# Kernel optimization log

Hardware: AMD Instinct MI355X
Metric: run time of the kernel (lower is better)

The kernel has to match this reference:

```python
import jax, jax.numpy as jnp
import numpy as np

LOOKUP_WINDOW = 101
OUTPUT_DIM = 128
NUM_BINS = 512


def setup_inputs() -> dict:
    key = jax.random.key(0)
    k1, k2 = jax.random.split(key)
    frames = jax.random.randint(k1, (16, 100, 27, 48, 3), 0, 256, dtype=jnp.int32)
    fc_w = jax.random.normal(k2, (LOOKUP_WINDOW, OUTPUT_DIM), dtype=jnp.float32) * 0.05
    fc_b = jnp.zeros((OUTPUT_DIM,), dtype=jnp.float32)
    return {"frames": frames, "fc_w": fc_w, "fc_b": fc_b}


def _color_histograms(frames):
    # frames: [B, T, H, W, 3] int32 in [0, 256)
    B, T, H, W, C = frames.shape
    f = frames.reshape(B * T, H * W, 3)
    R, G, Bc = f[:, :, 0], f[:, :, 1], f[:, :, 2]
    # 3 bits per channel -> 512 bins
    bins = ((R >> 5) << 6) + ((G >> 5) << 3) + (Bc >> 5)  # [BT, HW]
    frame_prefix = (jnp.arange(B * T, dtype=jnp.int32) << 9)[:, None]
    ids = (bins + frame_prefix).reshape(-1)
    hist = jax.ops.segment_sum(
        jnp.ones_like(ids, dtype=jnp.int32), ids,
        num_segments=B * T * NUM_BINS)
    hist = hist.reshape(B, T, NUM_BINS).astype(jnp.float32)
    # L2-normalize each frame's histogram
    hist = hist / jnp.linalg.norm(hist, axis=2, keepdims=True)
    return hist


def reference(frames, fc_w, fc_b):
    B, T = frames.shape[0], frames.shape[1]
    x = _color_histograms(frames)                  # [B, T, 512]
    sim = jnp.einsum('btd,bsd->bts', x, x)         # [B, T, T]
    half = (LOOKUP_WINDOW - 1) // 2
    padded = jnp.pad(sim, ((0, 0), (0, 0), (half, half)))  # [B, T, T+lw-1]
    # banded gather: band[b, t, w] = padded[b, t, t + w]
    idx = jnp.arange(T)[:, None] + jnp.arange(LOOKUP_WINDOW)[None, :]  # [T, lw]
    band = jnp.take_along_axis(
        padded, jnp.broadcast_to(idx[None], (B, T, LOOKUP_WINDOW)), axis=2)
    # Dense + relu
    return jax.nn.relu(band @ fc_w + fc_b)         # [B, T, 128]
```

## Files before the change

kernel.cpp:

```cpp
#include <hip/hip_runtime.h>
#include <hip/hip_bf16.h>
#include <math.h>

#define B_DIM 16
#define T_DIM 100
#define TPAD 112
#define HW_PIX (27 * 48)
#define NBINS 512
#define WIN 101
#define HALF 50
#define ODIM 128
#define NTILE 7
#define BSTRIDE 104

typedef __attribute__((ext_vector_type(8))) short s16x8;
typedef __attribute__((ext_vector_type(4))) float f32x4;

__global__ __launch_bounds__(256) void hist_kernel(
    const int* __restrict__ frames, __hip_bfloat16* __restrict__ X16) {
  const int bid = blockIdx.x;
  const int tid = threadIdx.x;

  if (bid >= B_DIM * T_DIM) {
    const int pid = bid - B_DIM * T_DIM;
    const int b = pid / (TPAD - T_DIM);
    const int r = pid - b * (TPAD - T_DIM);
    unsigned int* row = (unsigned int*)(X16 + ((size_t)(b * TPAD + T_DIM + r)) * NBINS);
    row[tid] = 0u;
    return;
  }

  __shared__ int h[NBINS];
  __shared__ float red[16];

  for (int i = tid; i < NBINS; i += 256) h[i] = 0;
  __syncthreads();

  const int* fp = frames + (size_t)bid * (HW_PIX * 3);
  for (int i = tid; i < HW_PIX / 4; i += 256) {
    const int4* q = (const int4*)(fp + 12 * i);
    int4 a = q[0], c = q[1], e = q[2];
    int b0 = ((a.x >> 5) << 6) + ((a.y >> 5) << 3) + (a.z >> 5);
    int b1 = ((a.w >> 5) << 6) + ((c.x >> 5) << 3) + (c.y >> 5);
    int b2 = ((c.z >> 5) << 6) + ((c.w >> 5) << 3) + (e.x >> 5);
    int b3 = ((e.y >> 5) << 6) + ((e.z >> 5) << 3) + (e.w >> 5);
    atomicAdd(&h[b0], 1);
    atomicAdd(&h[b1], 1);
    atomicAdd(&h[b2], 1);
    atomicAdd(&h[b3], 1);
  }
  __syncthreads();

  float ss = 0.f;
  for (int i = tid; i < NBINS; i += 256) {
    float v = (float)h[i];
    ss += v * v;
  }
  const int lane = tid & 63, wave = tid >> 6;
#pragma unroll
  for (int off = 32; off > 0; off >>= 1) ss += __shfl_down(ss, off);
  if (lane == 0) red[wave] = ss;
  __syncthreads();
  if (tid == 0) red[8] = 1.0f / sqrtf(red[0] + red[1] + red[2] + red[3]);
  __syncthreads();
  const float rn = red[8];

  const int b = bid / T_DIM;
  const int t = bid - b * T_DIM;
  __hip_bfloat16* row = X16 + ((size_t)(b * TPAD + t)) * NBINS;
  for (int i = tid; i < NBINS; i += 256) row[i] = __float2bfloat16((float)h[i] * rn);
}

__global__ __launch_bounds__(64) void sim_kernel(
    const __hip_bfloat16* __restrict__ X16, float* __restrict__ sim) {
  const int bid = blockIdx.x;
  const int b = bid / (NTILE * NTILE);
  const int tile = bid - b * (NTILE * NTILE);
  const int tm = tile / NTILE, tn = tile - tm * NTILE;
  const int lane = threadIdx.x;
  const int m16 = lane & 15, quad = lane >> 4;

  const short* A = (const short*)(X16 + ((size_t)(b * TPAD + tm * 16 + m16)) * NBINS) + quad * 8;
  const short* Bp = (const short*)(X16 + ((size_t)(b * TPAD + tn * 16 + m16)) * NBINS) + quad * 8;

  f32x4 acc = {0.f, 0.f, 0.f, 0.f};
#pragma unroll 4
  for (int k = 0; k < NBINS; k += 32) {
    s16x8 af = *(const s16x8*)(A + k);
    s16x8 bf = *(const s16x8*)(Bp + k);
    acc = __builtin_amdgcn_mfma_f32_16x16x32_bf16(af, bf, acc, 0, 0, 0);
  }

  const int n = tn * 16 + m16;
  if (n < T_DIM) {
    float* srow = sim + (size_t)b * T_DIM * T_DIM + n;
#pragma unroll
    for (int r = 0; r < 4; ++r) {
      int m = tm * 16 + quad * 4 + r;
      if (m < T_DIM) srow[(size_t)m * T_DIM] = acc[r];
    }
  }
}

__global__ __launch_bounds__(256) void band_fc_kernel(
    const float* __restrict__ sim, const float* __restrict__ fc_w,
    const float* __restrict__ fc_b, float* __restrict__ out) {
  __shared__ __align__(16) float wlds[WIN * ODIM];
  __shared__ float blds[16 * BSTRIDE];

  const int cid = blockIdx.x;
  const int b = cid / NTILE;
  const int t0 = (cid - b * NTILE) * 16;
  const int tid = threadIdx.x;

  {
    const f32x4* src = (const f32x4*)fc_w;
    f32x4* dst = (f32x4*)wlds;
    for (int i = tid; i < (WIN * ODIM) / 4; i += 256) dst[i] = src[i];
  }
  for (int idx = tid; idx < 16 * WIN; idx += 256) {
    int tl = idx / WIN;
    int j = idx - tl * WIN;
    int t = t0 + tl;
    int s = t - HALF + j;
    float v = 0.f;
    if (t < T_DIM && s >= 0 && s < T_DIM)
      v = sim[((size_t)b * T_DIM + t) * T_DIM + s];
    blds[tl * BSTRIDE + j] = v;
  }
  __syncthreads();

  const int g4 = tid & 31;
  const int tl0 = tid >> 5;
  const int tl1 = tl0 + 8;

  f32x4 acc0 = ((const f32x4*)fc_b)[g4];
  f32x4 acc1 = acc0;
#pragma unroll 4
  for (int j = 0; j < WIN; ++j) {
    f32x4 wv = *(const f32x4*)&wlds[j * ODIM + g4 * 4];
    float b0 = blds[tl0 * BSTRIDE + j];
    float b1 = blds[tl1 * BSTRIDE + j];
    acc0 += wv * b0;
    acc1 += wv * b1;
  }

#pragma unroll
  for (int c = 0; c < 4; ++c) {
    acc0[c] = fmaxf(acc0[c], 0.f);
    acc1[c] = fmaxf(acc1[c], 0.f);
  }

  const int t0a = t0 + tl0, t0b = t0 + tl1;
  if (t0a < T_DIM)
    *(f32x4*)&out[(((size_t)b * T_DIM + t0a)) * ODIM + g4 * 4] = acc0;
  if (t0b < T_DIM)
    *(f32x4*)&out[(((size_t)b * T_DIM + t0b)) * ODIM + g4 * 4] = acc1;
}

extern "C" void kernel_launch(void* const* d_in, const int* in_sizes, int n_in,
                              void* d_out, int out_size, void* d_ws, size_t ws_size,
                              hipStream_t stream) {
  const int* frames = (const int*)d_in[0];
  const float* fc_w = (const float*)d_in[1];
  const float* fc_b = (const float*)d_in[2];
  float* out = (float*)d_out;

  __hip_bfloat16* X16 = (__hip_bfloat16*)d_ws;
  float* sim = (float*)((char*)d_ws + (size_t)B_DIM * TPAD * NBINS * 2);

  hist_kernel<<<B_DIM * T_DIM + B_DIM * (TPAD - T_DIM), 256, 0, stream>>>(frames, X16);
  sim_kernel<<<B_DIM * NTILE * NTILE, 64, 0, stream>>>(X16, sim);
  band_fc_kernel<<<B_DIM * NTILE, 256, 0, stream>>>(sim, fc_w, fc_b, out);
}
```

Baseline: 88.32 us.

## Fuse similarity MFMA into banded FC kernel, computing only band tiles

```diff
diff --git a/kernel.cpp b/kernel.cpp
--- a/kernel.cpp
+++ b/kernel.cpp
@@ -10,8 +10,8 @@
 #define WIN 101
 #define HALF 50
 #define ODIM 128
-#define NTILE 7
-#define BSTRIDE 104
+#define NCHUNK 7
+#define SSTR 132
 
 typedef __attribute__((ext_vector_type(8))) short s16x8;
 typedef __attribute__((ext_vector_type(4))) float f32x4;
@@ -71,76 +71,66 @@
   for (int i = tid; i < NBINS; i += 256) row[i] = __float2bfloat16((float)h[i] * rn);
 }
 
-__global__ __launch_bounds__(64) void sim_kernel(
-    const __hip_bfloat16* __restrict__ X16, float* __restrict__ sim) {
-  const int bid = blockIdx.x;
-  const int b = bid / (NTILE * NTILE);
-  const int tile = bid - b * (NTILE * NTILE);
-  const int tm = tile / NTILE, tn = tile - tm * NTILE;
-  const int lane = threadIdx.x;
-  const int m16 = lane & 15, quad = lane >> 4;
-
-  const short* A = (const short*)(X16 + ((size_t)(b * TPAD + tm * 16 + m16)) * NBINS) + quad * 8;
-  const short* Bp = (const short*)(X16 + ((size_t)(b * TPAD + tn * 16 + m16)) * NBINS) + quad * 8;
-
-  f32x4 acc = {0.f, 0.f, 0.f, 0.f};
-#pragma unroll 4
-  for (int k = 0; k < NBINS; k += 32) {
-    s16x8 af = *(const s16x8*)(A + k);
-    s16x8 bf = *(const s16x8*)(Bp + k);
-    acc = __builtin_amdgcn_mfma_f32_16x16x32_bf16(af, bf, acc, 0, 0, 0);
-  }
-
-  const int n = tn * 16 + m16;
-  if (n < T_DIM) {
-    float* srow = sim + (size_t)b * T_DIM * T_DIM + n;
-#pragma unroll
-    for (int r = 0; r < 4; ++r) {
-      int m = tm * 16 + quad * 4 + r;
-      if (m < T_DIM) srow[(size_t)m * T_DIM] = acc[r];
-    }
-  }
-}
-
-__global__ __launch_bounds__(256) void band_fc_kernel(
-    const float* __restrict__ sim, const float* __restrict__ fc_w,
+__global__ __launch_bounds__(256) void simband_fc_kernel(
+    const __hip_bfloat16* __restrict__ X16, const float* __restrict__ fc_w,
     const float* __restrict__ fc_b, float* __restrict__ out) {
   __shared__ __align__(16) float wlds[WIN * ODIM];
-  __shared__ float blds[16 * BSTRIDE];
+  __shared__ float slds[16 * SSTR];
 
   const int cid = blockIdx.x;
-  const int b = cid / NTILE;
-  const int t0 = (cid - b * NTILE) * 16;
+  const int b = cid / NCHUNK;
+  const int t0 = (cid - b * NCHUNK) * 16;
+  const int s0 = t0 - HALF;
   const int tid = threadIdx.x;
+  const int lane = tid & 63, w = tid >> 6;
+  const int m16 = lane & 15, quad = lane >> 4;
 
   {
     const f32x4* src = (const f32x4*)fc_w;
     f32x4* dst = (f32x4*)wlds;
     for (int i = tid; i < (WIN * ODIM) / 4; i += 256) dst[i] = src[i];
   }
-  for (int idx = tid; idx < 16 * WIN; idx += 256) {
-    int tl = idx / WIN;
-    int j = idx - tl * WIN;
-    int t = t0 + tl;
-    int s = t - HALF + j;
-    float v = 0.f;
-    if (t < T_DIM && s >= 0 && s < T_DIM)
-      v = sim[((size_t)b * T_DIM + t) * T_DIM + s];
-    blds[tl * BSTRIDE + j] = v;
+
+  {
+    const int c0 = 2 * w;
+    const short* A = (const short*)(X16 + ((size_t)(b * TPAD + t0 + m16)) * NBINS) + quad * 8;
+    int sa = s0 + c0 * 16 + m16;
+    int sb = sa + 16;
+    sa = min(max(sa, 0), TPAD - 1);
+    sb = min(max(sb, 0), TPAD - 1);
+    const short* B0 = (const short*)(X16 + ((size_t)(b * TPAD + sa)) * NBINS) + quad * 8;
+    const short* B1 = (const short*)(X16 + ((size_t)(b * TPAD + sb)) * NBINS) + quad * 8;
+
+    f32x4 acc0 = {0.f, 0.f, 0.f, 0.f};
+    f32x4 acc1 = {0.f, 0.f, 0.f, 0.f};
+#pragma unroll 4
+    for (int k = 0; k < NBINS; k += 32) {
+      s16x8 af = *(const s16x8*)(A + k);
+      acc0 = __builtin_amdgcn_mfma_f32_16x16x32_bf16(af, *(const s16x8*)(B0 + k), acc0, 0, 0, 0);
+      acc1 = __builtin_amdgcn_mfma_f32_16x16x32_bf16(af, *(const s16x8*)(B1 + k), acc1, 0, 0, 0);
+    }
+#pragma unroll
+    for (int r = 0; r < 4; ++r) {
+      slds[(quad * 4 + r) * SSTR + c0 * 16 + m16] = acc0[r];
+      slds[(quad * 4 + r) * SSTR + (c0 + 1) * 16 + m16] = acc1[r];
+    }
   }
   __syncthreads();
 
   const int g4 = tid & 31;
   const int tl0 = tid >> 5;
   const int tl1 = tl0 + 8;
+  const int t_a = t0 + tl0, t_b = t0 + tl1;
+  const int jlo0 = max(0, HALF - t_a), jhi0 = min(WIN, HALF + T_DIM - t_a);
+  const int jlo1 = max(0, HALF - t_b), jhi1 = min(WIN, HALF + T_DIM - t_b);
 
   f32x4 acc0 = ((const f32x4*)fc_b)[g4];
   f32x4 acc1 = acc0;
 #pragma unroll 4
   for (int j = 0; j < WIN; ++j) {
     f32x4 wv = *(const f32x4*)&wlds[j * ODIM + g4 * 4];
-    float b0 = blds[tl0 * BSTRIDE + j];
-    float b1 = blds[tl1 * BSTRIDE + j];
+    float b0 = (j >= jlo0 && j < jhi0) ? slds[tl0 * SSTR + tl0 + j] : 0.f;
+    float b1 = (j >= jlo1 && j < jhi1) ? slds[tl1 * SSTR + tl1 + j] : 0.f;
     acc0 += wv * b0;
     acc1 += wv * b1;
   }
@@ -151,11 +141,10 @@
     acc1[c] = fmaxf(acc1[c], 0.f);
   }
 
-  const int t0a = t0 + tl0, t0b = t0 + tl1;
-  if (t0a < T_DIM)
-    *(f32x4*)&out[(((size_t)b * T_DIM + t0a)) * ODIM + g4 * 4] = acc0;
-  if (t0b < T_DIM)
-    *(f32x4*)&out[(((size_t)b * T_DIM + t0b)) * ODIM + g4 * 4] = acc1;
+  if (t_a < T_DIM)
+    *(f32x4*)&out[(((size_t)b * T_DIM + t_a)) * ODIM + g4 * 4] = acc0;
+  if (t_b < T_DIM)
+    *(f32x4*)&out[(((size_t)b * T_DIM + t_b)) * ODIM + g4 * 4] = acc1;
 }
 
 extern "C" void kernel_launch(void* const* d_in, const int* in_sizes, int n_in,
@@ -167,9 +156,7 @@
   float* out = (float*)d_out;
 
   __hip_bfloat16* X16 = (__hip_bfloat16*)d_ws;
-  float* sim = (float*)((char*)d_ws + (size_t)B_DIM * TPAD * NBINS * 2);
 
   hist_kernel<<<B_DIM * T_DIM + B_DIM * (TPAD - T_DIM), 256, 0, stream>>>(frames, X16);
-  sim_kernel<<<B_DIM * NTILE * NTILE, 64, 0, stream>>>(X16, sim);
-  band_fc_kernel<<<B_DIM * NTILE, 256, 0, stream>>>(sim, fc_w, fc_b, out);
+  simband_fc_kernel<<<B_DIM * NCHUNK, 256, 0, stream>>>(X16, fc_w, fc_b, out);
 }
```

Result: no change. 89.60 us (+1.4%).
